# Performance work log

Hardware: AMD Instinct MI355X
Metric: run time of the kernel (lower is better)

Reference implementation:

```python
import jax, jax.numpy as jnp
import numpy as np

N_NODES = 50000
N_EDGES = 800000
IN_CH = 128
HID = 64
OUT_CH = 2
NEG_SLOPE = 0.2


def gcn_conv(x, src, dst, deg_isqrt, W, b):
    # PyG GCNConv: x @ W, symmetric normalization with self-loops, scatter-add, + bias
    h = x @ W  # [N, HID]
    norm = deg_isqrt[src] * deg_isqrt[dst]  # [E+N]
    msg = h[src] * norm[:, None]  # gather + scale
    out = jax.ops.segment_sum(msg, dst, num_segments=x.shape[0])
    return out + b


def setup_inputs() -> dict:
    key = jax.random.key(0)
    ks = jax.random.split(key, 16)
    glorot = lambda k, i, o: jax.random.normal(k, (i, o), jnp.float32) * jnp.sqrt(2.0 / (i + o))
    inp = {
        "node_features": jax.random.normal(ks[0], (N_NODES, IN_CH), jnp.float32),
        "edge_index": jax.random.randint(ks[1], (2, N_EDGES), 0, N_NODES, jnp.int64 if jax.config.jax_enable_x64 else jnp.int32),
        "fc1_W": glorot(ks[2], IN_CH, 32), "fc1_b": jnp.zeros((32,), jnp.float32),
        "fc2_W": glorot(ks[3], 32, HID), "fc2_b": jnp.zeros((HID,), jnp.float32),
        "conv1_W": glorot(ks[4], HID, HID), "conv1_b": jnp.zeros((HID,), jnp.float32),
        "conv2_W": glorot(ks[5], HID, HID), "conv2_b": jnp.zeros((HID,), jnp.float32),
        "conv3_W": glorot(ks[6], HID, HID), "conv3_b": jnp.zeros((HID,), jnp.float32),
        "conv4_W": glorot(ks[7], HID, HID), "conv4_b": jnp.zeros((HID,), jnp.float32),
        "final_W": glorot(ks[8], HID, OUT_CH), "final_b": jnp.zeros((OUT_CH,), jnp.float32),
    }
    return inp


def reference(node_features, edge_index, fc1_W, fc1_b, fc2_W, fc2_b,
              conv1_W, conv1_b, conv2_W, conv2_b, conv3_W, conv3_b,
              conv4_W, conv4_b, final_W, final_b):
    N = node_features.shape[0]
    # add self-loops once (shared by all conv layers)
    loops = jnp.arange(N, dtype=edge_index.dtype)
    src = jnp.concatenate([edge_index[0], loops])
    dst = jnp.concatenate([edge_index[1], loops])
    deg = jax.ops.segment_sum(jnp.ones_like(dst, jnp.float32), dst, num_segments=N)
    deg_isqrt = jnp.where(deg > 0, jax.lax.rsqrt(jnp.maximum(deg, 1.0)), 0.0)

    lrelu = lambda x: jnp.where(x >= 0, x, NEG_SLOPE * x)

    x = jax.nn.relu(node_features @ fc1_W + fc1_b) @ fc2_W + fc2_b  # fc stack
    out1 = lrelu(gcn_conv(x, src, dst, deg_isqrt, conv1_W, conv1_b))
    out2 = lrelu(gcn_conv(out1, src, dst, deg_isqrt, conv2_W, conv2_b)) + out1
    out3 = lrelu(gcn_conv(out2, src, dst, deg_isqrt, conv3_W, conv3_b))
    out4 = gcn_conv(out3, src, dst, deg_isqrt, conv4_W, conv4_b) + out2
    return out4 @ final_W + final_b
```

## Files before the change

### kernel.cpp

```cpp
#include <hip/hip_runtime.h>

#define NN 50000
#define NHALF 25000
#define NE 800000
#define HIST_BLOCKS ((NE + 255) / 256)
#define FILL_BLOCKS HIST_BLOCKS
#define FC_BLOCKS 1024

typedef unsigned short u16;
typedef unsigned int u32;

__device__ inline float rlf(float v, int l) {
    return __int_as_float(__builtin_amdgcn_readlane(__float_as_int(v), l));
}
__device__ inline u16 f2bf(float f) {
    u32 u = __float_as_uint(f);
    u32 r = (u + 0x7FFFu + ((u >> 16) & 1u)) >> 16;
    return (u16)r;
}
__device__ inline float lo16(u32 q) { return __uint_as_float(q << 16); }
__device__ inline float hi16(u32 q) { return __uint_as_float(q & 0xffff0000u); }

__global__ __launch_bounds__(256) void k_hist_foldw(
    const int* __restrict__ dst, int* __restrict__ cnt,
    const float* __restrict__ fc2W, const float* __restrict__ b2,
    const float* __restrict__ c1W, float* __restrict__ W2c,
    float* __restrict__ b2c) {
    if (blockIdx.x < HIST_BLOCKS) {
        int e = blockIdx.x * 256 + threadIdx.x;
        if (e < NE) atomicAdd(&cnt[dst[e]], 1);
    } else {
        int j = (blockIdx.x - HIST_BLOCKS) * 4 + (threadIdx.x >> 6);
        int c = threadIdx.x & 63;
        if (j < 32) {
            float s = 0.f;
            for (int k = 0; k < 64; ++k) s = fmaf(fc2W[j * 64 + k], c1W[k * 64 + c], s);
            W2c[j * 64 + c] = s;
        } else if (j == 32) {
            float s = 0.f;
            for (int k = 0; k < 64; ++k) s = fmaf(b2[k], c1W[k * 64 + c], s);
            b2c[c] = s;
        }
    }
}

__global__ __launch_bounds__(1024) void k_scan(int* __restrict__ cnt,
                                               int* __restrict__ rowptr,
                                               float* __restrict__ disq,
                                               u16* __restrict__ Hb) {
    __shared__ int wsum[16];
    __shared__ int carry;
    int t = threadIdx.x, wave = t >> 6, lane = t & 63;
    if (t == 0) { carry = 0; rowptr[0] = 0; }
    if (t < 64) Hb[(size_t)NN * 64 + t] = 0;
    __syncthreads();
    for (int base = 0; base < NN; base += 1024) {
        int i = base + t;
        int x = (i < NN) ? cnt[i] : 0;
        if (i < NN) {
            cnt[i] = 0;
            disq[i] = rsqrtf((float)x + 1.0f);
        }
        for (int off = 1; off < 64; off <<= 1) {
            int y = __shfl_up(x, off, 64);
            if (lane >= off) x += y;
        }
        if (lane == 63) wsum[wave] = x;
        __syncthreads();
        if (wave == 0 && lane < 16) {
            int w = wsum[lane];
            for (int off = 1; off < 16; off <<= 1) {
                int y = __shfl_up(w, off, 16);
                if (lane >= off) w += y;
            }
            wsum[lane] = w;
        }
        __syncthreads();
        int incl = carry + ((wave > 0) ? wsum[wave - 1] : 0) + x;
        if (i < NN) rowptr[i + 1] = incl;
        __syncthreads();
        if (t == 1023) carry = incl;
        __syncthreads();
    }
}

__global__ __launch_bounds__(256) void k_fill_fc(
    const int* __restrict__ src, const int* __restrict__ dst,
    const int* __restrict__ rowptr, int* __restrict__ cur,
    u16* __restrict__ esrc,
    const float* __restrict__ nf,
    const float* __restrict__ W1, const float* __restrict__ b1,
    const float* __restrict__ W2c, const float* __restrict__ b2c,
    const float* __restrict__ disq, u16* __restrict__ Hb) {
    if (blockIdx.x >= FC_BLOCKS) {
        int e = (blockIdx.x - FC_BLOCKS) * 256 + threadIdx.x;
        if (e < NE) {
            int d = dst[e];
            int pos = rowptr[d] + atomicAdd(&cur[d], 1);
            esrc[pos] = (u16)src[e];
        }
        return;
    }
    int lane = threadIdx.x & 63;
    int c = lane & 31, h = lane >> 5;
    int wid = (blockIdx.x * 256 + threadIdx.x) >> 6;
    int nwaves = (FC_BLOCKS * 256) >> 6;
    float w1[64], w2[32];
    #pragma unroll
    for (int j = 0; j < 64; ++j) w1[j] = W1[(h * 64 + j) * 32 + c];
    #pragma unroll
    for (int j = 0; j < 32; ++j) w2[j] = W2c[j * 64 + lane];
    float b1c = b1[c], b2l = b2c[lane];
    for (int n = wid; n < NN; n += nwaves) {
        float x0 = nf[(size_t)n * 128 + lane];
        float x1 = nf[(size_t)n * 128 + 64 + lane];
        float s = 0.f;
        #pragma unroll
        for (int j = 0; j < 64; ++j) {
            float xa = rlf(x0, j), xb = rlf(x1, j);
            s = fmaf(h ? xb : xa, w1[j], s);
        }
        s += __shfl_xor(s, 32, 64);
        float hv = fmaxf(s + b1c, 0.f);
        float o = b2l;
        #pragma unroll
        for (int j = 0; j < 32; ++j) o = fmaf(rlf(hv, j), w2[j], o);
        Hb[(size_t)n * 64 + lane] = f2bf(disq[n] * o);
    }
}

__global__ __launch_bounds__(256) void k_gemm64(
    const float* __restrict__ X, const float* __restrict__ W,
    const float* __restrict__ disq, u16* __restrict__ Hb) {
    int lane = threadIdx.x & 63;
    int wid = (blockIdx.x * 256 + threadIdx.x) >> 6;
    int nwaves = (gridDim.x * 256) >> 6;
    float wcol[64];
    #pragma unroll
    for (int k = 0; k < 64; ++k) wcol[k] = W[k * 64 + lane];
    for (int n = wid; n < NN; n += nwaves) {
        float xv = X[(size_t)n * 64 + lane];
        float acc = 0.f;
        #pragma unroll
        for (int k = 0; k < 64; ++k) acc = fmaf(rlf(xv, k), wcol[k], acc);
        Hb[(size_t)n * 64 + lane] = f2bf(disq[n] * acc);
    }
}

#define GRPA(J)                                                             \
    {                                                                       \
        int p0 = __builtin_amdgcn_readlane(idx1, (J) + 0);                  \
        int p1 = __builtin_amdgcn_readlane(idx1, (J) + 1);                  \
        int p2 = __builtin_amdgcn_readlane(idx1, (J) + 2);                  \
        int p3 = __builtin_amdgcn_readlane(idx1, (J) + 3);                  \
        int s = (q == 0) ? p0 : ((q == 1) ? p1 : ((q == 2) ? p2 : p3));     \
        uint2 v = *(const uint2*)(Hb + (((size_t)s) << 6) + c4);            \
        a0 += lo16(v.x); a1 += hi16(v.x); a2 += lo16(v.y); a3 += hi16(v.y); \
    }
#define GRPB(J)                                                             \
    {                                                                       \
        int p0 = __builtin_amdgcn_readlane(idx2, (J) + 0);                  \
        int p1 = __builtin_amdgcn_readlane(idx2, (J) + 1);                  \
        int p2 = __builtin_amdgcn_readlane(idx2, (J) + 2);                  \
        int p3 = __builtin_amdgcn_readlane(idx2, (J) + 3);                  \
        int s = (q == 0) ? p0 : ((q == 1) ? p1 : ((q == 2) ? p2 : p3));     \
        uint2 v = *(const uint2*)(Hb + (((size_t)s) << 6) + c4);            \
        g0 += lo16(v.x); g1 += hi16(v.x); g2 += lo16(v.y); g3 += hi16(v.y); \
    }

__global__ __launch_bounds__(256) void k_csr_conv(
    const u16* __restrict__ Hb, const int* __restrict__ rowptr,
    const u16* __restrict__ esrc, const float* __restrict__ disq,
    const float* __restrict__ b, const float* __restrict__ res,
    float* __restrict__ out, int do_lrelu) {
    int lane = threadIdx.x & 63;
    int q = lane >> 4;
    int c4 = (lane & 15) * 4;
    int w = (blockIdx.x * 256 + threadIdx.x) >> 6;
    if (w >= NHALF) return;
    int n1 = w, n2 = w + NHALF;
    int base1 = rowptr[n1], end1 = rowptr[n1 + 1];
    int base2 = rowptr[n2], end2 = rowptr[n2 + 1];
    float a0 = 0.f, a1 = 0.f, a2 = 0.f, a3 = 0.f;
    float g0 = 0.f, g1 = 0.f, g2 = 0.f, g3 = 0.f;
    while (base1 < end1 || base2 < end2) {
        int m1 = min(max(end1 - base1, 0), 64);
        int m2 = min(max(end2 - base2, 0), 64);
        int idx1 = (lane < m1) ? (int)esrc[base1 + lane] : NN;
        int idx2 = (lane < m2) ? (int)esrc[base2 + lane] : NN;
        int m = max(m1, m2);
        int j = 0;
        for (; j + 16 <= m; j += 16) {
            GRPA(j) GRPB(j) GRPA(j + 4) GRPB(j + 4)
            GRPA(j + 8) GRPB(j + 8) GRPA(j + 12) GRPB(j + 12)
        }
        for (; j < m; j += 4) { GRPA(j) GRPB(j) }
        base1 += 64;
        base2 += 64;
    }
    a0 += __shfl_xor(a0, 16, 64); a0 += __shfl_xor(a0, 32, 64);
    a1 += __shfl_xor(a1, 16, 64); a1 += __shfl_xor(a1, 32, 64);
    a2 += __shfl_xor(a2, 16, 64); a2 += __shfl_xor(a2, 32, 64);
    a3 += __shfl_xor(a3, 16, 64); a3 += __shfl_xor(a3, 32, 64);
    g0 += __shfl_xor(g0, 16, 64); g0 += __shfl_xor(g0, 32, 64);
    g1 += __shfl_xor(g1, 16, 64); g1 += __shfl_xor(g1, 32, 64);
    g2 += __shfl_xor(g2, 16, 64); g2 += __shfl_xor(g2, 32, 64);
    g3 += __shfl_xor(g3, 16, 64); g3 += __shfl_xor(g3, 32, 64);
    if (q < 2) {
        int n = (q == 0) ? n1 : n2;
        float e0 = (q == 0) ? a0 : g0;
        float e1 = (q == 0) ? a1 : g1;
        float e2 = (q == 0) ? a2 : g2;
        float e3 = (q == 0) ? a3 : g3;
        uint2 sv = *(const uint2*)(Hb + (((size_t)n) << 6) + c4);
        e0 += lo16(sv.x); e1 += hi16(sv.x); e2 += lo16(sv.y); e3 += hi16(sv.y);
        float dn = disq[n];
        float4 bv = *(const float4*)(b + c4);
        float v0 = dn * e0 + bv.x;
        float v1 = dn * e1 + bv.y;
        float v2 = dn * e2 + bv.z;
        float v3 = dn * e3 + bv.w;
        if (do_lrelu) {
            v0 = (v0 >= 0.f) ? v0 : 0.2f * v0;
            v1 = (v1 >= 0.f) ? v1 : 0.2f * v1;
            v2 = (v2 >= 0.f) ? v2 : 0.2f * v2;
            v3 = (v3 >= 0.f) ? v3 : 0.2f * v3;
        }
        if (res) {
            float4 r = *(const float4*)(res + (((size_t)n) << 6) + c4);
            v0 += r.x; v1 += r.y; v2 += r.z; v3 += r.w;
        }
        float4 o;
        o.x = v0; o.y = v1; o.z = v2; o.w = v3;
        *(float4*)(out + (((size_t)n) << 6) + c4) = o;
    }
}

__global__ __launch_bounds__(256) void k_csr_conv_final(
    const u16* __restrict__ Hb, const int* __restrict__ rowptr,
    const u16* __restrict__ esrc, const float* __restrict__ disq,
    const float* __restrict__ b, const float* __restrict__ res,
    const float* __restrict__ FW, const float* __restrict__ fb,
    float* __restrict__ out) {
    int lane = threadIdx.x & 63;
    int q = lane >> 4;
    int c4 = (lane & 15) * 4;
    int w = (blockIdx.x * 256 + threadIdx.x) >> 6;
    if (w >= NHALF) return;
    int n1 = w, n2 = w + NHALF;
    int base1 = rowptr[n1], end1 = rowptr[n1 + 1];
    int base2 = rowptr[n2], end2 = rowptr[n2 + 1];
    float a0 = 0.f, a1 = 0.f, a2 = 0.f, a3 = 0.f;
    float g0 = 0.f, g1 = 0.f, g2 = 0.f, g3 = 0.f;
    while (base1 < end1 || base2 < end2) {
        int m1 = min(max(end1 - base1, 0), 64);
        int m2 = min(max(end2 - base2, 0), 64);
        int idx1 = (lane < m1) ? (int)esrc[base1 + lane] : NN;
        int idx2 = (lane < m2) ? (int)esrc[base2 + lane] : NN;
        int m = max(m1, m2);
        int j = 0;
        for (; j + 16 <= m; j += 16) {
            GRPA(j) GRPB(j) GRPA(j + 4) GRPB(j + 4)
            GRPA(j + 8) GRPB(j + 8) GRPA(j + 12) GRPB(j + 12)
        }
        for (; j < m; j += 4) { GRPA(j) GRPB(j) }
        base1 += 64;
        base2 += 64;
    }
    a0 += __shfl_xor(a0, 16, 64); a0 += __shfl_xor(a0, 32, 64);
    a1 += __shfl_xor(a1, 16, 64); a1 += __shfl_xor(a1, 32, 64);
    a2 += __shfl_xor(a2, 16, 64); a2 += __shfl_xor(a2, 32, 64);
    a3 += __shfl_xor(a3, 16, 64); a3 += __shfl_xor(a3, 32, 64);
    g0 += __shfl_xor(g0, 16, 64); g0 += __shfl_xor(g0, 32, 64);
    g1 += __shfl_xor(g1, 16, 64); g1 += __shfl_xor(g1, 32, 64);
    g2 += __shfl_xor(g2, 16, 64); g2 += __shfl_xor(g2, 32, 64);
    g3 += __shfl_xor(g3, 16, 64); g3 += __shfl_xor(g3, 32, 64);
    float p0 = 0.f, p1 = 0.f;
    int n = (q == 0) ? n1 : n2;
    if (q < 2) {
        float e0 = (q == 0) ? a0 : g0;
        float e1 = (q == 0) ? a1 : g1;
        float e2 = (q == 0) ? a2 : g2;
        float e3 = (q == 0) ? a3 : g3;
        uint2 sv = *(const uint2*)(Hb + (((size_t)n) << 6) + c4);
        e0 += lo16(sv.x); e1 += hi16(sv.x); e2 += lo16(sv.y); e3 += hi16(sv.y);
        float dn = disq[n];
        float4 bv = *(const float4*)(b + c4);
        float4 r = *(const float4*)(res + (((size_t)n) << 6) + c4);
        float v0 = dn * e0 + bv.x + r.x;
        float v1 = dn * e1 + bv.y + r.y;
        float v2 = dn * e2 + bv.z + r.z;
        float v3 = dn * e3 + bv.w + r.w;
        float4 f01 = *(const float4*)(FW + c4 * 2);
        float4 f23 = *(const float4*)(FW + c4 * 2 + 4);
        p0 = v0 * f01.x + v1 * f01.z + v2 * f23.x + v3 * f23.z;
        p1 = v0 * f01.y + v1 * f01.w + v2 * f23.y + v3 * f23.w;
    }
    for (int off = 1; off < 16; off <<= 1) {
        p0 += __shfl_xor(p0, off, 64);
        p1 += __shfl_xor(p1, off, 64);
    }
    if (lane == 0 || lane == 16) {
        out[n * 2 + 0] = p0 + fb[0];
        out[n * 2 + 1] = p1 + fb[1];
    }
}

extern "C" void kernel_launch(void* const* d_in, const int* in_sizes, int n_in,
                              void* d_out, int out_size, void* d_ws, size_t ws_size,
                              hipStream_t stream) {
    const float* nf   = (const float*)d_in[0];
    const int*   ei   = (const int*)d_in[1];
    const float* fc1W = (const float*)d_in[2];
    const float* fc1b = (const float*)d_in[3];
    const float* fc2W = (const float*)d_in[4];
    const float* fc2b = (const float*)d_in[5];
    const float* cW[4] = {(const float*)d_in[6], (const float*)d_in[8],
                          (const float*)d_in[10], (const float*)d_in[12]};
    const float* cb[4] = {(const float*)d_in[7], (const float*)d_in[9],
                          (const float*)d_in[11], (const float*)d_in[13]};
    const float* fW = (const float*)d_in[14];
    const float* fb = (const float*)d_in[15];
    const int* src = ei;
    const int* dst = ei + NE;

    float* ws     = (float*)d_ws;
    float* disq   = ws;
    int*   cnt    = (int*)(ws + 50048);
    int*   rowptr = cnt + 50048;
    u16*   esrc   = (u16*)(rowptr + 50056);
    float* W2c    = (float*)(esrc + 800064);
    float* b2c    = W2c + 2048;
    float* B0     = b2c + 64;
    float* B1     = B0 + (size_t)NN * 64;
    u16*   Hb     = (u16*)(B1 + (size_t)NN * 64);

    hipMemsetAsync(cnt, 0, 50048 * sizeof(int), stream);
    k_hist_foldw<<<HIST_BLOCKS + 9, 256, 0, stream>>>(dst, cnt, fc2W, fc2b, cW[0],
                                                      W2c, b2c);
    k_scan<<<1, 1024, 0, stream>>>(cnt, rowptr, disq, Hb);
    k_fill_fc<<<FC_BLOCKS + FILL_BLOCKS, 256, 0, stream>>>(
        src, dst, rowptr, cnt, esrc, nf, fc1W, fc1b, W2c, b2c, disq, Hb);

    const int cgrid = (NHALF * 64 + 255) / 256;

    k_csr_conv<<<cgrid, 256, 0, stream>>>(Hb, rowptr, esrc, disq, cb[0], nullptr, B1, 1);
    k_gemm64<<<512, 256, 0, stream>>>(B1, cW[1], disq, Hb);
    k_csr_conv<<<cgrid, 256, 0, stream>>>(Hb, rowptr, esrc, disq, cb[1], B1, B0, 1);
    k_gemm64<<<512, 256, 0, stream>>>(B0, cW[2], disq, Hb);
    k_csr_conv<<<cgrid, 256, 0, stream>>>(Hb, rowptr, esrc, disq, cb[2], nullptr, B1, 1);
    k_gemm64<<<512, 256, 0, stream>>>(B1, cW[3], disq, Hb);
    k_csr_conv_final<<<cgrid, 256, 0, stream>>>(Hb, rowptr, esrc, disq, cb[3], B0,
                                                fW, fb, (float*)d_out);
}
```

Measured before the change: 314.6 us.

## Pair nodes of equal degree per wave via degree-sorted permutation in CSR conv

```diff
diff --git a/kernel.cpp b/kernel.cpp
--- a/kernel.cpp
+++ b/kernel.cpp
@@ -6,6 +6,7 @@
 #define HIST_BLOCKS ((NE + 255) / 256)
 #define FILL_BLOCKS HIST_BLOCKS
 #define FC_BLOCKS 1024
+#define PERM_BLOCKS ((NN + 255) / 256)
 
 typedef unsigned short u16;
 typedef unsigned int u32;
@@ -47,12 +48,16 @@
 __global__ __launch_bounds__(1024) void k_scan(int* __restrict__ cnt,
                                                int* __restrict__ rowptr,
                                                float* __restrict__ disq,
-                                               u16* __restrict__ Hb) {
+                                               u16* __restrict__ Hb,
+                                               int* __restrict__ dbase,
+                                               int* __restrict__ dcur) {
     __shared__ int wsum[16];
     __shared__ int carry;
+    __shared__ int dh[256];
     int t = threadIdx.x, wave = t >> 6, lane = t & 63;
     if (t == 0) { carry = 0; rowptr[0] = 0; }
     if (t < 64) Hb[(size_t)NN * 64 + t] = 0;
+    if (t < 256) dh[t] = 0;
     __syncthreads();
     for (int base = 0; base < NN; base += 1024) {
         int i = base + t;
@@ -60,6 +65,7 @@
         if (i < NN) {
             cnt[i] = 0;
             disq[i] = rsqrtf((float)x + 1.0f);
+            atomicAdd(&dh[min(x, 255)], 1);
         }
         for (int off = 1; off < 64; off <<= 1) {
             int y = __shfl_up(x, off, 64);
@@ -82,6 +88,17 @@
         if (t == 1023) carry = incl;
         __syncthreads();
     }
+    for (int off = 1; off < 256; off <<= 1) {
+        int v = 0;
+        if (t < 256 && t >= off) v = dh[t - off];
+        __syncthreads();
+        if (t < 256) dh[t] += v;
+        __syncthreads();
+    }
+    if (t < 256) {
+        dbase[t] = NN - dh[t];
+        dcur[t] = 0;
+    }
 }
 
 __global__ __launch_bounds__(256) void k_fill_fc(
@@ -91,7 +108,17 @@
     const float* __restrict__ nf,
     const float* __restrict__ W1, const float* __restrict__ b1,
     const float* __restrict__ W2c, const float* __restrict__ b2c,
-    const float* __restrict__ disq, u16* __restrict__ Hb) {
+    const float* __restrict__ disq, u16* __restrict__ Hb,
+    int* __restrict__ dbase, int* __restrict__ dcur, u16* __restrict__ perm) {
+    if (blockIdx.x >= FC_BLOCKS + FILL_BLOCKS) {
+        int i = (blockIdx.x - FC_BLOCKS - FILL_BLOCKS) * 256 + threadIdx.x;
+        if (i < NN) {
+            int d = min(rowptr[i + 1] - rowptr[i], 255);
+            int pos = dbase[d] + atomicAdd(&dcur[d], 1);
+            perm[pos] = (u16)i;
+        }
+        return;
+    }
     if (blockIdx.x >= FC_BLOCKS) {
         int e = (blockIdx.x - FC_BLOCKS) * 256 + threadIdx.x;
         if (e < NE) {
@@ -114,18 +141,24 @@
     for (int n = wid; n < NN; n += nwaves) {
         float x0 = nf[(size_t)n * 128 + lane];
         float x1 = nf[(size_t)n * 128 + 64 + lane];
-        float s = 0.f;
+        float s0 = 0.f, s1 = 0.f;
         #pragma unroll
-        for (int j = 0; j < 64; ++j) {
+        for (int j = 0; j < 32; ++j) {
             float xa = rlf(x0, j), xb = rlf(x1, j);
-            s = fmaf(h ? xb : xa, w1[j], s);
-        }
+            float xc = rlf(x0, j + 32), xd = rlf(x1, j + 32);
+            s0 = fmaf(h ? xb : xa, w1[j], s0);
+            s1 = fmaf(h ? xd : xc, w1[j + 32], s1);
+        }
+        float s = s0 + s1;
         s += __shfl_xor(s, 32, 64);
         float hv = fmaxf(s + b1c, 0.f);
-        float o = b2l;
+        float o0 = b2l, o1 = 0.f;
         #pragma unroll
-        for (int j = 0; j < 32; ++j) o = fmaf(rlf(hv, j), w2[j], o);
-        Hb[(size_t)n * 64 + lane] = f2bf(disq[n] * o);
+        for (int j = 0; j < 16; ++j) {
+            o0 = fmaf(rlf(hv, j), w2[j], o0);
+            o1 = fmaf(rlf(hv, j + 16), w2[j + 16], o1);
+        }
+        Hb[(size_t)n * 64 + lane] = f2bf(disq[n] * (o0 + o1));
     }
 }
 
@@ -170,7 +203,8 @@
 
 __global__ __launch_bounds__(256) void k_csr_conv(
     const u16* __restrict__ Hb, const int* __restrict__ rowptr,
-    const u16* __restrict__ esrc, const float* __restrict__ disq,
+    const u16* __restrict__ esrc, const u16* __restrict__ perm,
+    const float* __restrict__ disq,
     const float* __restrict__ b, const float* __restrict__ res,
     float* __restrict__ out, int do_lrelu) {
     int lane = threadIdx.x & 63;
@@ -178,7 +212,7 @@
     int c4 = (lane & 15) * 4;
     int w = (blockIdx.x * 256 + threadIdx.x) >> 6;
     if (w >= NHALF) return;
-    int n1 = w, n2 = w + NHALF;
+    int n1 = perm[2 * w], n2 = perm[2 * w + 1];
     int base1 = rowptr[n1], end1 = rowptr[n1 + 1];
     int base2 = rowptr[n2], end2 = rowptr[n2 + 1];
     float a0 = 0.f, a1 = 0.f, a2 = 0.f, a3 = 0.f;
@@ -238,7 +272,8 @@
 
 __global__ __launch_bounds__(256) void k_csr_conv_final(
     const u16* __restrict__ Hb, const int* __restrict__ rowptr,
-    const u16* __restrict__ esrc, const float* __restrict__ disq,
+    const u16* __restrict__ esrc, const u16* __restrict__ perm,
+    const float* __restrict__ disq,
     const float* __restrict__ b, const float* __restrict__ res,
     const float* __restrict__ FW, const float* __restrict__ fb,
     float* __restrict__ out) {
@@ -247,7 +282,7 @@
     int c4 = (lane & 15) * 4;
     int w = (blockIdx.x * 256 + threadIdx.x) >> 6;
     if (w >= NHALF) return;
-    int n1 = w, n2 = w + NHALF;
+    int n1 = perm[2 * w], n2 = perm[2 * w + 1];
     int base1 = rowptr[n1], end1 = rowptr[n1 + 1];
     int base2 = rowptr[n2], end2 = rowptr[n2 + 1];
     float a0 = 0.f, a1 = 0.f, a2 = 0.f, a3 = 0.f;
@@ -329,7 +364,10 @@
     int*   cnt    = (int*)(ws + 50048);
     int*   rowptr = cnt + 50048;
     u16*   esrc   = (u16*)(rowptr + 50056);
-    float* W2c    = (float*)(esrc + 800064);
+    u16*   perm   = esrc + 800000;
+    int*   dbase  = (int*)(perm + 50048);
+    int*   dcur   = dbase + 256;
+    float* W2c    = (float*)(dcur + 256);
     float* b2c    = W2c + 2048;
     float* B0     = b2c + 64;
     float* B1     = B0 + (size_t)NN * 64;
@@ -338,18 +376,22 @@
     hipMemsetAsync(cnt, 0, 50048 * sizeof(int), stream);
     k_hist_foldw<<<HIST_BLOCKS + 9, 256, 0, stream>>>(dst, cnt, fc2W, fc2b, cW[0],
                                                       W2c, b2c);
-    k_scan<<<1, 1024, 0, stream>>>(cnt, rowptr, disq, Hb);
-    k_fill_fc<<<FC_BLOCKS + FILL_BLOCKS, 256, 0, stream>>>(
-        src, dst, rowptr, cnt, esrc, nf, fc1W, fc1b, W2c, b2c, disq, Hb);
+    k_scan<<<1, 1024, 0, stream>>>(cnt, rowptr, disq, Hb, dbase, dcur);
+    k_fill_fc<<<FC_BLOCKS + FILL_BLOCKS + PERM_BLOCKS, 256, 0, stream>>>(
+        src, dst, rowptr, cnt, esrc, nf, fc1W, fc1b, W2c, b2c, disq, Hb,
+        dbase, dcur, perm);
 
     const int cgrid = (NHALF * 64 + 255) / 256;
 
-    k_csr_conv<<<cgrid, 256, 0, stream>>>(Hb, rowptr, esrc, disq, cb[0], nullptr, B1, 1);
+    k_csr_conv<<<cgrid, 256, 0, stream>>>(Hb, rowptr, esrc, perm, disq, cb[0],
+                                          nullptr, B1, 1);
     k_gemm64<<<512, 256, 0, stream>>>(B1, cW[1], disq, Hb);
-    k_csr_conv<<<cgrid, 256, 0, stream>>>(Hb, rowptr, esrc, disq, cb[1], B1, B0, 1);
+    k_csr_conv<<<cgrid, 256, 0, stream>>>(Hb, rowptr, esrc, perm, disq, cb[1],
+                                          B1, B0, 1);
     k_gemm64<<<512, 256, 0, stream>>>(B0, cW[2], disq, Hb);
-    k_csr_conv<<<cgrid, 256, 0, stream>>>(Hb, rowptr, esrc, disq, cb[2], nullptr, B1, 1);
+    k_csr_conv<<<cgrid, 256, 0, stream>>>(Hb, rowptr, esrc, perm, disq, cb[2],
+                                          nullptr, B1, 1);
     k_gemm64<<<512, 256, 0, stream>>>(B1, cW[3], disq, Hb);
-    k_csr_conv_final<<<cgrid, 256, 0, stream>>>(Hb, rowptr, esrc, disq, cb[3], B0,
-                                                fW, fb, (float*)d_out);
-}
+    k_csr_conv_final<<<cgrid, 256, 0, stream>>>(Hb, rowptr, esrc, perm, disq, cb[3],
+                                                B0, fW, fb, (float*)d_out);
+}
```

Measured after the change: 459.4 us. +46.1%, slower.
